# Kernel tuning notes

Hardware: AMD Instinct MI355X
Metric: run time of the kernel (lower is better)

The kernel has to match this reference:

```python
import jax, jax.numpy as jnp
import numpy as np

B, M, N_CTR, K = 16, 2048, 512, 32
DIM, DEPTH, HEADS = 384, 6, 6
EMB = 48  # fourier embedding dim (48//6 = 8 freqs per axis, basis [3,24])


def make_basis():
    e = (2.0 ** np.arange(EMB // 6)).astype(np.float32) * np.pi  # [8]
    z = np.zeros(EMB // 6, np.float32)
    basis = np.stack([np.concatenate([e, z, z]),
                      np.concatenate([z, e, z]),
                      np.concatenate([z, z, e])])  # [3, 24]
    return jnp.asarray(basis)


def fourier_embed(x, basis):
    # x [..., 3] -> [..., 48]  (sin/cos of 24 frequency projections)
    p = jnp.einsum('...d,de->...e', x, basis)
    return jnp.concatenate([jnp.sin(p), jnp.cos(p)], axis=-1)


def fps_idx(pos, n):
    # farthest point sampling, deterministic start at index 0. pos [M,3] -> [n]
    d0 = jnp.sum((pos - pos[0]) ** 2, -1)
    def step(d, _):
        i = jnp.argmax(d)
        d = jnp.minimum(d, jnp.sum((pos - pos[i]) ** 2, -1))
        return d, i
    _, idxs = jax.lax.scan(step, d0, None, length=n - 1)
    return jnp.concatenate([jnp.zeros(1, jnp.int32), idxs.astype(jnp.int32)])


def layernorm(x, g, b, eps=1e-6):
    m = jnp.mean(x, -1, keepdims=True)
    v = jnp.var(x, -1, keepdims=True)
    return (x - m) * jax.lax.rsqrt(v + eps) * g + b


def _lin(key, fi, fo):
    kw, kb = jax.random.split(key)
    w = jax.random.normal(kw, (fi, fo), jnp.float32) / np.sqrt(fi)
    b = jax.random.normal(kb, (fo,), jnp.float32) * 0.01
    return w, b


def setup_inputs() -> dict:
    key = jax.random.key(0)
    ks = jax.random.split(key, 16)
    pc = jax.random.uniform(ks[0], (B, M, 3), jnp.float32)
    embed_w, embed_b = _lin(ks[1], 3 + EMB, DIM)
    lw1, lb1 = _lin(ks[2], 3 + EMB, 256)
    lw2, lb2 = _lin(ks[3], 256, 256)
    gw1, gb1 = _lin(ks[4], 256, 256)
    gw2, gb2 = _lin(ks[5], 256, DIM)
    def stack_lin(k, fi, fo):
        kk = jax.random.split(k, DEPTH)
        ws, bs = zip(*[_lin(kk[i], fi, fo) for i in range(DEPTH)])
        return jnp.stack(ws), jnp.stack(bs)
    qkv_w, qkv_b = stack_lin(ks[6], DIM, 3 * DIM)
    proj_w, proj_b = stack_lin(ks[7], DIM, DIM)
    fc1_w, fc1_b = stack_lin(ks[8], DIM, 4 * DIM)
    fc2_w, fc2_b = stack_lin(ks[9], 4 * DIM, DIM)
    return dict(
        pc=pc, embed_w=embed_w, embed_b=embed_b,
        lw1=lw1, lb1=lb1, lw2=lw2, lb2=lb2,
        gw1=gw1, gb1=gb1, gw2=gw2, gb2=gb2,
        ln1_g=jnp.ones((DEPTH, DIM)), ln1_b=jnp.zeros((DEPTH, DIM)),
        qkv_w=qkv_w, qkv_b=qkv_b, proj_w=proj_w, proj_b=proj_b,
        gamma1=jax.random.normal(ks[10], (DEPTH, DIM)) * 0.1,
        ln2_g=jnp.ones((DEPTH, DIM)), ln2_b=jnp.zeros((DEPTH, DIM)),
        fc1_w=fc1_w, fc1_b=fc1_b, fc2_w=fc2_w, fc2_b=fc2_b,
        gamma2=jax.random.normal(ks[11], (DEPTH, DIM)) * 0.1,
        lnf_g=jnp.ones((DIM,)), lnf_b=jnp.zeros((DIM,)),
    )


def reference(pc, embed_w, embed_b, lw1, lb1, lw2, lb2, gw1, gb1, gw2, gb2,
              ln1_g, ln1_b, qkv_w, qkv_b, proj_w, proj_b, gamma1,
              ln2_g, ln2_b, fc1_w, fc1_b, fc2_w, fc2_b, gamma2, lnf_g, lnf_b):
    basis = make_basis()
    # --- FPS centers (per batch) ---
    idx = jax.vmap(lambda p: fps_idx(p, N_CTR))(pc)                 # [B,N]
    centers = jnp.take_along_axis(pc, idx[:, :, None], axis=1)      # [B,N,3]
    # --- KNN graph: for each center, K nearest of the M points ---
    d2 = jnp.sum((centers[:, :, None, :] - pc[:, None, :, :]) ** 2, -1)  # [B,N,M]
    _, nn_idx = jax.lax.top_k(-d2, K)                               # [B,N,K]
    # --- PointConv: gather -> local MLP -> max-scatter -> global MLP ---
    src = jax.vmap(lambda p, i: p[i])(pc, nn_idx)                   # [B,N,K,3]
    rel = src - centers[:, :, None, :]
    feat = jnp.concatenate([rel, fourier_embed(rel, basis)], -1)    # [B,N,K,51]
    h = jax.nn.relu(feat @ lw1 + lb1) @ lw2 + lb2                   # [B,N,K,256]
    h = jnp.max(h, axis=2)  # scatter_max over edges == max over K neighbors
    x = jax.nn.relu(h @ gw1 + gb1) @ gw2 + gb2                      # [B,N,DIM]
    # --- positional embedding tokens ---
    pe = jnp.concatenate([centers, fourier_embed(centers, basis)], -1) @ embed_w + embed_b
    x = x + pe
    # --- ViT blocks (pre-LN, LayerScale, eval mode: no dropout/droppath) ---
    hd = DIM // HEADS
    scale = hd ** -0.5
    for l in range(DEPTH):
        xn = layernorm(x, ln1_g[l], ln1_b[l])
        qkv = (xn @ qkv_w[l] + qkv_b[l]).reshape(B, N_CTR, 3, HEADS, hd)
        q, k, v = jnp.moveaxis(qkv, 2, 0)                           # [B,N,H,hd]
        att = jax.nn.softmax(jnp.einsum('bqhd,bkhd->bhqk', q, k) * scale, axis=-1)
        o = jnp.einsum('bhqk,bkhd->bqhd', att, v).reshape(B, N_CTR, DIM)
        x = x + gamma1[l] * (o @ proj_w[l] + proj_b[l])
        xn = layernorm(x, ln2_g[l], ln2_b[l])
        mlp = jax.nn.gelu(xn @ fc1_w[l] + fc1_b[l], approximate=False) @ fc2_w[l] + fc2_b[l]
        x = x + gamma2[l] * mlp
    out = layernorm(x, lnf_g, lnf_b)
    return out, centers
```

## Files before the change

### kernel.cpp

```cpp
#include <hip/hip_runtime.h>
#include <math.h>

#define NB 16
#define NM 2048
#define NCTR 512
#define NK 32
#define NDIM 384

typedef unsigned long long ull;
typedef unsigned int uint;
typedef unsigned short ushort;
typedef __attribute__((ext_vector_type(8))) short bf16x8;
typedef __attribute__((ext_vector_type(4))) float f32x4;

__device__ __forceinline__ float dist2_exact(float ax, float ay, float az,
                                             float bx, float by, float bz) {
  float dx = __fsub_rn(ax, bx);
  float dy = __fsub_rn(ay, by);
  float dz = __fsub_rn(az, bz);
  return __fadd_rn(__fadd_rn(__fmul_rn(dx, dx), __fmul_rn(dy, dy)),
                   __fmul_rn(dz, dz));
}

__device__ __forceinline__ float gelu_f(float x) {
  return 0.5f * x * (1.0f + erff(x * 0.70710678118654752f));
}

__device__ __forceinline__ ushort f2bf(float f) {
  uint u = __float_as_uint(f);
  return (ushort)((u + 0x7FFFu + ((u >> 16) & 1u)) >> 16);
}
__device__ __forceinline__ float bf2f(ushort h) {
  return __uint_as_float(((uint)h) << 16);
}

__device__ __forceinline__ void cvt8(float4 p, float4 q, uint4& hi, uint4& lo) {
  float v0 = p.x, v1 = p.y, v2 = p.z, v3 = p.w;
  float v4 = q.x, v5 = q.y, v6 = q.z, v7 = q.w;
  ushort h0 = f2bf(v0), h1 = f2bf(v1), h2 = f2bf(v2), h3 = f2bf(v3);
  ushort h4 = f2bf(v4), h5 = f2bf(v5), h6 = f2bf(v6), h7 = f2bf(v7);
  ushort l0 = f2bf(v0 - bf2f(h0)), l1 = f2bf(v1 - bf2f(h1));
  ushort l2 = f2bf(v2 - bf2f(h2)), l3 = f2bf(v3 - bf2f(h3));
  ushort l4 = f2bf(v4 - bf2f(h4)), l5 = f2bf(v5 - bf2f(h5));
  ushort l6 = f2bf(v6 - bf2f(h6)), l7 = f2bf(v7 - bf2f(h7));
  hi.x = (uint)h0 | ((uint)h1 << 16); hi.y = (uint)h2 | ((uint)h3 << 16);
  hi.z = (uint)h4 | ((uint)h5 << 16); hi.w = (uint)h6 | ((uint)h7 << 16);
  lo.x = (uint)l0 | ((uint)l1 << 16); lo.y = (uint)l2 | ((uint)l3 << 16);
  lo.z = (uint)l4 | ((uint)l5 << 16); lo.w = (uint)l6 | ((uint)l7 << 16);
}

__device__ __forceinline__ void split_store(float v, ushort* H, ushort* L,
                                            size_t off) {
  ushort hi = f2bf(v);
  H[off] = hi;
  L[off] = f2bf(v - bf2f(hi));
}

__device__ __forceinline__ void gload16(const ushort* g, ushort* l) {
  __builtin_amdgcn_global_load_lds(
      (const __attribute__((address_space(1))) void*)g,
      (__attribute__((address_space(3))) void*)l, 16, 0, 0);
}

__global__ __launch_bounds__(256)
void fps_kernel(const float* __restrict__ pc, float* __restrict__ centers) {
  int b = blockIdx.x;
  __shared__ float4 pos4[NM];
  __shared__ ull red[2][4];
  const float* pb = pc + (size_t)b * (NM * 3);
  int tid = threadIdx.x, lane = tid & 63, wv = tid >> 6;
  float px[8], py[8], pz[8];
#pragma unroll
  for (int i = 0; i < 8; ++i) {
    int p = tid + 256 * i;
    float x = pb[3 * p], y = pb[3 * p + 1], z = pb[3 * p + 2];
    px[i] = x; py[i] = y; pz[i] = z;
    pos4[p] = make_float4(x, y, z, 0.f);
  }
  __syncthreads();
  float* cb = centers + (size_t)b * (NCTR * 3);
  float4 s0 = pos4[0];
  float sx = s0.x, sy = s0.y, sz = s0.z;
  if (tid == 0) { cb[0] = sx; cb[1] = sy; cb[2] = sz; }
  float d[8];
  for (int n = 1; n < NCTR; ++n) {
    ull best = 0;
#pragma unroll
    for (int i = 0; i < 8; ++i) {
      int p = tid + 256 * i;
      float nd = dist2_exact(px[i], py[i], pz[i], sx, sy, sz);
      d[i] = (n == 1) ? nd : fminf(d[i], nd);
      ull key = ((ull)__float_as_uint(d[i]) << 32) | (unsigned)(0x7FFFFFFF - p);
      best = best > key ? best : key;
    }
    float dl = __uint_as_float((uint)(best >> 32));
    float wm = dl;
#pragma unroll
    for (int off = 32; off; off >>= 1) wm = fmaxf(wm, __shfl_xor(wm, off));
    ull mask = __ballot(dl == wm);
    ull wkey;
    if (mask & (mask - 1)) {
      wkey = best;
#pragma unroll
      for (int off = 32; off; off >>= 1) {
        ull o = __shfl_xor(wkey, off);
        wkey = wkey > o ? wkey : o;
      }
    } else {
      int src = __ffsll((long long)mask) - 1;
      wkey = __shfl(best, src);
    }
    if (lane == 0) red[n & 1][wv] = wkey;
    __syncthreads();
    ull g0 = red[n & 1][0], g1 = red[n & 1][1];
    ull g2 = red[n & 1][2], g3 = red[n & 1][3];
    ull ga = g0 > g1 ? g0 : g1;
    ull gc2 = g2 > g3 ? g2 : g3;
    ull gb = ga > gc2 ? ga : gc2;
    int j = 0x7FFFFFFF - (int)(unsigned)(gb & 0xFFFFFFFFull);
    float4 np = pos4[j];
    sx = np.x; sy = np.y; sz = np.z;
    if (tid == 0) { cb[n * 3] = sx; cb[n * 3 + 1] = sy; cb[n * 3 + 2] = sz; }
  }
}

__global__ __launch_bounds__(256, 2)
void knn_kernel(const float* __restrict__ pc, const float* __restrict__ centers,
                int* __restrict__ nn) {
  __shared__ float pos[NM * 3];
  int b = blockIdx.x >> 7;
  int n0 = (blockIdx.x & 127) << 2;
  const float* pb = pc + (size_t)b * (NM * 3);
  for (int i = threadIdx.x; i < NM * 3; i += 256) pos[i] = pb[i];
  __syncthreads();
  int wv = threadIdx.x >> 6, lane = threadIdx.x & 63;
  int gc = b * NCTR + n0 + wv;
  float cx = centers[gc * 3], cy = centers[gc * 3 + 1], cz = centers[gc * 3 + 2];
  ull key[32];
  ull gmin[4];
#pragma unroll
  for (int g = 0; g < 4; ++g) {
    gmin[g] = ~0ull;
#pragma unroll
    for (int i = 0; i < 8; ++i) {
      int r = g * 8 + i;
      int p = lane + (r << 6);
      float nd = dist2_exact(pos[3 * p], pos[3 * p + 1], pos[3 * p + 2], cx, cy, cz);
      key[r] = ((ull)__float_as_uint(nd) << 11) | (unsigned)p;
      gmin[g] = gmin[g] < key[r] ? gmin[g] : key[r];
    }
  }
  ull a01 = gmin[0] < gmin[1] ? gmin[0] : gmin[1];
  ull a23 = gmin[2] < gmin[3] ? gmin[2] : gmin[3];
  ull lmin = a01 < a23 ? a01 : a23;
  int* nnc = nn + (size_t)gc * NK;
  for (int round = 0; round < NK; ++round) {
    ull w = lmin;
#pragma unroll
    for (int off = 32; off; off >>= 1) {
      ull o = __shfl_xor(w, off);
      w = w < o ? w : o;
    }
    if (lmin == w) {
      nnc[round] = (int)(w & 2047ull);
#pragma unroll
      for (int g = 0; g < 4; ++g) {
        if (gmin[g] == w) {
          gmin[g] = ~0ull;
#pragma unroll
          for (int i = 0; i < 8; ++i) {
            int r = g * 8 + i;
            key[r] = (key[r] == w) ? ~0ull : key[r];
            gmin[g] = gmin[g] < key[r] ? gmin[g] : key[r];
          }
        }
      }
      ull b01 = gmin[0] < gmin[1] ? gmin[0] : gmin[1];
      ull b23 = gmin[2] < gmin[3] ? gmin[2] : gmin[3];
      lmin = b01 < b23 ? b01 : b23;
    }
  }
}

struct WAll {
  const float* src[8];
  ushort* dst[8];
  int K8[8];
  int N[8];
  int Ksrc[8];
  int blk0[9];
};

__global__ __launch_bounds__(256)
void wconv8(WAll a) {
  int bid = blockIdx.x;
  int f = 0;
#pragma unroll
  for (int i = 1; i < 8; ++i) f += (bid >= a.blk0[i]);
  int K8 = a.K8[f], N = a.N[f], Ksrc = a.Ksrc[f];
  int c = (bid - a.blk0[f]) * 256 + threadIdx.x;
  if (c >= K8 * N) return;
  const float* W = a.src[f];
  ushort* out = a.dst[f];
  int kb = c / N, n = c - kb * N;
  float v[8];
#pragma unroll
  for (int i = 0; i < 8; ++i) {
    int row = kb * 8 + i;
    v[i] = (row < Ksrc) ? W[(size_t)row * N + n] : 0.f;
  }
  float4 p, q;
  p.x = v[0]; p.y = v[1]; p.z = v[2]; p.w = v[3];
  q.x = v[4]; q.y = v[5]; q.z = v[6]; q.w = v[7];
  uint4 hi, lo;
  cvt8(p, q, hi, lo);
  *(uint4*)(out + (size_t)c * 8) = hi;
  *(uint4*)(out + (size_t)(K8 * N + c) * 8) = lo;
}

__global__ __launch_bounds__(256, 2)
void edge_mfma(const float* __restrict__ pc, const float* __restrict__ centers,
               const int* __restrict__ nn, const ushort* __restrict__ lw1s,
               const float* __restrict__ lb1, const ushort* __restrict__ lw2s,
               const float* __restrict__ lb2, ushort* __restrict__ hH,
               ushort* __restrict__ hL) {
  __shared__ __align__(16) ushort featH[4096], featL[4096];
  __shared__ __align__(16) ushort t1H[16384], t1L[16384];
  int tid = threadIdx.x;
  int w = tid >> 6, lane = tid & 63;
  int l15 = lane & 15, l4 = lane >> 4;
  int wbase = w << 6;
  {
    int e = tid >> 2, s = tid & 3;
    int ge = blockIdx.x * 64 + e;
    int c = ge >> 5;
    int b = c >> 9;
    int j = nn[ge];
    const float* sp = pc + ((size_t)b * NM + j) * 3;
    float rx = sp[0] - centers[c * 3];
    float ry = sp[1] - centers[c * 3 + 1];
    float rz = sp[2] - centers[c * 3 + 2];
    auto putk = [&](int k, float v) {
      ushort hi = f2bf(v);
      ushort lo = f2bf(v - bf2f(hi));
      int idx = ((k >> 3) * 64 + e) * 8 + (k & 7);
      featH[idx] = hi;
      featL[idx] = lo;
    };
    if (s < 3) {
      float r = (s == 0) ? rx : (s == 1) ? ry : rz;
#pragma unroll
      for (int f = 0; f < 8; ++f) {
        float ef = (float)(M_PI * (double)(1 << f));
        float p = r * ef;
        putk(3 + 8 * s + f, sinf(p));
        putk(27 + 8 * s + f, cosf(p));
      }
    } else {
      putk(0, rx);
      putk(1, ry);
      putk(2, rz);
#pragma unroll
      for (int k = 51; k < 64; ++k) putk(k, 0.f);
    }
  }
  __syncthreads();
  const ushort* lw1H = lw1s;
  const ushort* lw1L = lw1s + 8 * 256 * 8;
  f32x4 acc1[4][4];
#pragma unroll
  for (int i = 0; i < 4; ++i)
#pragma unroll
    for (int j = 0; j < 4; ++j) acc1[i][j] = (f32x4){0.f, 0.f, 0.f, 0.f};
#pragma unroll
  for (int ks = 0; ks < 2; ++ks) {
    bf16x8 ah[4], al[4];
#pragma unroll
    for (int fm = 0; fm < 4; ++fm) {
      int idx = ((ks * 4 + l4) * 64 + fm * 16 + l15) * 8;
      ah[fm] = *(const bf16x8*)&featH[idx];
      al[fm] = *(const bf16x8*)&featL[idx];
    }
#pragma unroll
    for (int fn = 0; fn < 4; ++fn) {
      int col = wbase + fn * 16 + l15;
      size_t boff = ((size_t)(ks * 4 + l4) * 256 + col) * 8;
      bf16x8 bh = *(const bf16x8*)(lw1H + boff);
      bf16x8 bl = *(const bf16x8*)(lw1L + boff);
#pragma unroll
      for (int fm = 0; fm < 4; ++fm) {
        acc1[fm][fn] = __builtin_amdgcn_mfma_f32_16x16x32_bf16(al[fm], bh, acc1[fm][fn], 0, 0, 0);
        acc1[fm][fn] = __builtin_amdgcn_mfma_f32_16x16x32_bf16(ah[fm], bl, acc1[fm][fn], 0, 0, 0);
        acc1[fm][fn] = __builtin_amdgcn_mfma_f32_16x16x32_bf16(ah[fm], bh, acc1[fm][fn], 0, 0, 0);
      }
    }
  }
#pragma unroll
  for (int fn = 0; fn < 4; ++fn) {
    int chan = wbase + fn * 16 + l15;
    float bias = lb1[chan];
    int kb = chan >> 3, k7 = chan & 7;
#pragma unroll
    for (int fm = 0; fm < 4; ++fm) {
#pragma unroll
      for (int r = 0; r < 4; ++r) {
        int edge = fm * 16 + l4 * 4 + r;
        float v = fmaxf(acc1[fm][fn][r] + bias, 0.f);
        ushort hi = f2bf(v);
        ushort lo = f2bf(v - bf2f(hi));
        int idx = (kb * 64 + edge) * 8 + k7;
        t1H[idx] = hi;
        t1L[idx] = lo;
      }
    }
  }
  __syncthreads();
  const ushort* lw2H = lw2s;
  const ushort* lw2L = lw2s + 32 * 256 * 8;
  f32x4 acc2[4][4];
#pragma unroll
  for (int i = 0; i < 4; ++i)
#pragma unroll
    for (int j = 0; j < 4; ++j) acc2[i][j] = (f32x4){0.f, 0.f, 0.f, 0.f};
#pragma unroll
  for (int ks = 0; ks < 8; ++ks) {
    bf16x8 ah[4], al[4];
#pragma unroll
    for (int fm = 0; fm < 4; ++fm) {
      int idx = ((ks * 4 + l4) * 64 + fm * 16 + l15) * 8;
      ah[fm] = *(const bf16x8*)&t1H[idx];
      al[fm] = *(const bf16x8*)&t1L[idx];
    }
#pragma unroll
    for (int fn = 0; fn < 4; ++fn) {
      int col = wbase + fn * 16 + l15;
      size_t boff = ((size_t)(ks * 4 + l4) * 256 + col) * 8;
      bf16x8 bh = *(const bf16x8*)(lw2H + boff);
      bf16x8 bl = *(const bf16x8*)(lw2L + boff);
#pragma unroll
      for (int fm = 0; fm < 4; ++fm) {
        acc2[fm][fn] = __builtin_amdgcn_mfma_f32_16x16x32_bf16(al[fm], bh, acc2[fm][fn], 0, 0, 0);
        acc2[fm][fn] = __builtin_amdgcn_mfma_f32_16x16x32_bf16(ah[fm], bl, acc2[fm][fn], 0, 0, 0);
        acc2[fm][fn] = __builtin_amdgcn_mfma_f32_16x16x32_bf16(ah[fm], bh, acc2[fm][fn], 0, 0, 0);
      }
    }
  }
#pragma unroll
  for (int fn = 0; fn < 4; ++fn) {
    int col = wbase + fn * 16 + l15;
    float m0 = -INFINITY, m1 = -INFINITY;
#pragma unroll
    for (int r = 0; r < 4; ++r) {
      m0 = fmaxf(m0, fmaxf(acc2[0][fn][r], acc2[1][fn][r]));
      m1 = fmaxf(m1, fmaxf(acc2[2][fn][r], acc2[3][fn][r]));
    }
    m0 = fmaxf(m0, __shfl_xor(m0, 16));
    m0 = fmaxf(m0, __shfl_xor(m0, 32));
    m1 = fmaxf(m1, __shfl_xor(m1, 16));
    m1 = fmaxf(m1, __shfl_xor(m1, 32));
    if (l4 == 0) {
      float bias = lb2[col];
      int c0 = blockIdx.x * 2;
      split_store(m0 + bias, hH, hL, (size_t)c0 * 256 + col);
      split_store(m1 + bias, hH, hL, (size_t)(c0 + 1) * 256 + col);
    }
  }
}

template <int EPI, int OUTS, int BM>
__global__ __launch_bounds__(256, 2)
void gemm_s(const ushort* __restrict__ AH, const ushort* __restrict__ AL,
            const ushort* __restrict__ Wh, const ushort* __restrict__ Wl,
            const float* __restrict__ bias, const float* __restrict__ gamma,
            const float* __restrict__ resid, float* __restrict__ C,
            ushort* __restrict__ CH, ushort* __restrict__ CL,
            int M, int N, int K) {
  constexpr int WC = (BM == 128) ? 2 : 4;
  constexpr int FN = 128 / (WC * 16);
  constexpr int ACH = BM / 64;
  __shared__ __align__(16) ushort Ah[2][BM * 32], Al[2][BM * 32];
  __shared__ __align__(16) ushort Bh[2][4096], Bl[2][4096];
  int tid = threadIdx.x;
  int bn = blockIdx.x << 7, bm = blockIdx.y * BM;
  int wid = tid >> 6, lane = tid & 63;
  int wr = (BM == 128) ? (wid >> 1) : 0;
  int wc = (BM == 128) ? (wid & 1) : wid;
  int l15 = lane & 15, l4 = lane >> 4;

  f32x4 acc[4][FN];
#pragma unroll
  for (int i = 0; i < 4; ++i)
#pragma unroll
    for (int j = 0; j < FN; ++j) acc[i][j] = (f32x4){0.f, 0.f, 0.f, 0.f};

  auto stage = [&](int buf, int kt) {
#pragma unroll
    for (int q = 0; q < ACH; ++q) {
      int e = q * 256 + tid;
      int kb = e / BM, row = e % BM;
      size_t so = (size_t)(bm + row) * K + kt * 32 + kb * 8;
      gload16(AH + so, &Ah[buf][e * 8]);
      gload16(AL + so, &Al[buf][e * 8]);
    }
#pragma unroll
    for (int q = 0; q < 2; ++q) {
      int e = q * 256 + tid;
      int kb = e >> 7, n = e & 127;
      size_t so = ((size_t)(kt * 4 + kb) * N + bn + n) * 8;
      gload16(Wh + so, &Bh[buf][e * 8]);
      gload16(Wl + so, &Bl[buf][e * 8]);
    }
  };

  int nkt = K >> 5;
  stage(0, 0);
  for (int kt = 0; kt < nkt; ++kt) {
    int cur = kt & 1;
    __syncthreads();
    if (kt + 1 < nkt) stage(cur ^ 1, kt + 1);
    bf16x8 ahf[4], alf[4];
#pragma unroll
    for (int fm = 0; fm < 4; ++fm) {
      int ci = l4 * BM + wr * 64 + fm * 16 + l15;
      ahf[fm] = *(bf16x8*)&Ah[cur][ci * 8];
      alf[fm] = *(bf16x8*)&Al[cur][ci * 8];
    }
#pragma unroll
    for (int fn = 0; fn < FN; ++fn) {
      int ci = l4 * 128 + wc * (FN * 16) + fn * 16 + l15;
      bf16x8 bh = *(bf16x8*)&Bh[cur][ci * 8];
      bf16x8 bl = *(bf16x8*)&Bl[cur][ci * 8];
#pragma unroll
      for (int fm = 0; fm < 4; ++fm) {
        acc[fm][fn] = __builtin_amdgcn_mfma_f32_16x16x32_bf16(alf[fm], bh, acc[fm][fn], 0, 0, 0);
        acc[fm][fn] = __builtin_amdgcn_mfma_f32_16x16x32_bf16(ahf[fm], bl, acc[fm][fn], 0, 0, 0);
        acc[fm][fn] = __builtin_amdgcn_mfma_f32_16x16x32_bf16(ahf[fm], bh, acc[fm][fn], 0, 0, 0);
      }
    }
  }

#pragma unroll
  for (int fn = 0; fn < FN; ++fn) {
    int col = bn + wc * (FN * 16) + fn * 16 + l15;
    float bv = bias[col];
    float gv = (EPI == 3) ? gamma[col] : 0.f;
#pragma unroll
    for (int fm = 0; fm < 4; ++fm) {
      int row0 = bm + wr * 64 + fm * 16 + l4 * 4;
#pragma unroll
      for (int r = 0; r < 4; ++r) {
        float v = acc[fm][fn][r] + bv;
        if (EPI == 1) v = fmaxf(v, 0.f);
        else if (EPI == 2) v = gelu_f(v);
        else if (EPI == 3) v = resid[(size_t)(row0 + r) * N + col] + gv * v;
        size_t off = (size_t)(row0 + r) * N + col;
        if (OUTS == 0) C[off] = v;
        else split_store(v, CH, CL, off);
      }
    }
  }
}

__global__ __launch_bounds__(256)
void pe_add(const float* __restrict__ centers, const float* __restrict__ ew,
            const float* __restrict__ eb, float* x) {
  __shared__ float fc[51];
  int c = blockIdx.x, tid = threadIdx.x;
  if (tid < 24) {
    int a = tid >> 3, f = tid & 7;
    float coord = centers[c * 3 + a];
    float p = coord * (float)(M_PI * (double)(1 << f));
    fc[3 + tid] = sinf(p);
    fc[27 + tid] = cosf(p);
  } else if (tid < 27) {
    fc[tid - 24] = centers[c * 3 + (tid - 24)];
  }
  __syncthreads();
  for (int j = tid; j < NDIM; j += 256) {
    float acc = eb[j];
#pragma unroll
    for (int d = 0; d < 51; ++d) acc = fmaf(fc[d], ew[d * NDIM + j], acc);
    x[(size_t)c * NDIM + j] += acc;
  }
}

__global__ __launch_bounds__(256)
void ln_f32(const float* __restrict__ x, const float* __restrict__ g,
            const float* __restrict__ b, float* __restrict__ y) {
  int row = (blockIdx.x << 2) + (threadIdx.x >> 6);
  int lane = threadIdx.x & 63;
  const float* xr = x + (size_t)row * NDIM;
  float v[6];
#pragma unroll
  for (int i = 0; i < 6; ++i) v[i] = xr[lane + (i << 6)];
  float s = 0.f;
#pragma unroll
  for (int i = 0; i < 6; ++i) s += v[i];
#pragma unroll
  for (int off = 32; off; off >>= 1) s += __shfl_xor(s, off);
  float m = s / 384.f;
  float var = 0.f;
#pragma unroll
  for (int i = 0; i < 6; ++i) { float dd = v[i] - m; var += dd * dd; }
#pragma unroll
  for (int off = 32; off; off >>= 1) var += __shfl_xor(var, off);
  var = var / 384.f;
  float rs = 1.f / sqrtf(var + 1e-6f);
#pragma unroll
  for (int i = 0; i < 6; ++i) {
    int cc = lane + (i << 6);
    y[(size_t)row * NDIM + cc] = (v[i] - m) * rs * g[cc] + b[cc];
  }
}

__global__ __launch_bounds__(256)
void ln_split(const float* __restrict__ x, const float* __restrict__ g,
              const float* __restrict__ b, ushort* __restrict__ yH,
              ushort* __restrict__ yL) {
  int row = (blockIdx.x << 2) + (threadIdx.x >> 6);
  int lane = threadIdx.x & 63;
  const float* xr = x + (size_t)row * NDIM;
  float v[6];
#pragma unroll
  for (int i = 0; i < 6; ++i) v[i] = xr[lane + (i << 6)];
  float s = 0.f;
#pragma unroll
  for (int i = 0; i < 6; ++i) s += v[i];
#pragma unroll
  for (int off = 32; off; off >>= 1) s += __shfl_xor(s, off);
  float m = s / 384.f;
  float var = 0.f;
#pragma unroll
  for (int i = 0; i < 6; ++i) { float dd = v[i] - m; var += dd * dd; }
#pragma unroll
  for (int off = 32; off; off >>= 1) var += __shfl_xor(var, off);
  var = var / 384.f;
  float rs = 1.f / sqrtf(var + 1e-6f);
#pragma unroll
  for (int i = 0; i < 6; ++i) {
    int cc = lane + (i << 6);
    float yv = (v[i] - m) * rs * g[cc] + b[cc];
    split_store(yv, yH, yL, (size_t)row * NDIM + cc);
  }
}

__global__ __launch_bounds__(256, 2)
void attn_mfma(const ushort* __restrict__ FH, const ushort* __restrict__ FL,
               ushort* __restrict__ oH, ushort* __restrict__ oL) {
  __shared__ __align__(16) ushort kTH[4096], kTL[4096];
  __shared__ __align__(16) ushort vSH[4096], vSL[4096];
  __shared__ __align__(16) ushort pSH[8192], pSL[8192];
  int bi = blockIdx.x;
  int qt = bi & 3;
  int hh = (bi >> 2) % 6;
  int b = bi / 24;
  int tid = threadIdx.x;
  int w = tid >> 6, lane = tid & 63;
  int l15 = lane & 15, l4 = lane >> 4;
  const ushort* baseH = FH + (size_t)(b * NCTR) * 1152;
  const ushort* baseL = FL + (size_t)(b * NCTR) * 1152;
  int qbase = qt * 128 + w * 32;

  bf16x8 qh[2][2], ql[2][2];
#pragma unroll
  for (int qr = 0; qr < 2; ++qr) {
#pragma unroll
    for (int ds = 0; ds < 2; ++ds) {
      size_t off = (size_t)(qbase + qr * 16 + l15) * 1152 + hh * 64 + ds * 32 + l4 * 8;
      qh[qr][ds] = *(const bf16x8*)(baseH + off);
      ql[qr][ds] = *(const bf16x8*)(baseL + off);
    }
  }

  f32x4 oacc[2][4];
#pragma unroll
  for (int i = 0; i < 2; ++i)
#pragma unroll
    for (int j = 0; j < 4; ++j) oacc[i][j] = (f32x4){0.f, 0.f, 0.f, 0.f};
  float m_[2][4], l_[2][4];
#pragma unroll
  for (int i = 0; i < 2; ++i)
#pragma unroll
    for (int r = 0; r < 4; ++r) { m_[i][r] = -INFINITY; l_[i][r] = 0.f; }

  ushort* pHw = pSH + w * 2048;
  ushort* pLw = pSL + w * 2048;

  for (int ch = 0; ch < 8; ++ch) {
    {
      int key = tid & 63, dgh = tid >> 6;
      size_t krow = (size_t)(ch * 64 + key) * 1152 + 384 + hh * 64;
#pragma unroll
      for (int i = 0; i < 2; ++i) {
        int dg = dgh * 2 + i;
        *(uint4*)&kTH[(dg * 64 + key) * 8] = *(const uint4*)(baseH + krow + dg * 8);
        *(uint4*)&kTL[(dg * 64 + key) * 8] = *(const uint4*)(baseL + krow + dg * 8);
      }
      int d = tid & 63, kb2 = tid >> 6;
#pragma unroll
      for (int i = 0; i < 2; ++i) {
        int kb = kb2 + i * 4;
        ushort hv[8], lv[8];
#pragma unroll
        for (int j = 0; j < 8; ++j) {
          size_t off = (size_t)(ch * 64 + kb * 8 + j) * 1152 + 768 + hh * 64 + d;
          hv[j] = baseH[off];
          lv[j] = baseL[off];
        }
        uint4 H, L;
        H.x = (uint)hv[0] | ((uint)hv[1] << 16); H.y = (uint)hv[2] | ((uint)hv[3] << 16);
        H.z = (uint)hv[4] | ((uint)hv[5] << 16); H.w = (uint)hv[6] | ((uint)hv[7] << 16);
        L.x = (uint)lv[0] | ((uint)lv[1] << 16); L.y = (uint)lv[2] | ((uint)lv[3] << 16);
        L.z = (uint)lv[4] | ((uint)lv[5] << 16); L.w = (uint)lv[6] | ((uint)lv[7] << 16);
        *(uint4*)&vSH[(kb * 64 + d) * 8] = H;
        *(uint4*)&vSL[(kb * 64 + d) * 8] = L;
      }
    }
    __syncthreads();

    f32x4 sacc[2][4];
#pragma unroll
    for (int i = 0; i < 2; ++i)
#pragma unroll
      for (int j = 0; j < 4; ++j) sacc[i][j] = (f32x4){0.f, 0.f, 0.f, 0.f};
#pragma unroll
    for (int ds = 0; ds < 2; ++ds) {
#pragma unroll
      for (int kc = 0; kc < 4; ++kc) {
        int idx = ((ds * 4 + l4) * 64 + kc * 16 + l15) * 8;
        bf16x8 bh = *(const bf16x8*)&kTH[idx];
        bf16x8 bl = *(const bf16x8*)&kTL[idx];
#pragma unroll
        for (int qr = 0; qr < 2; ++qr) {
          sacc[qr][kc] = __builtin_amdgcn_mfma_f32_16x16x32_bf16(ql[qr][ds], bh, sacc[qr][kc], 0, 0, 0);
          sacc[qr][kc] = __builtin_amdgcn_mfma_f32_16x16x32_bf16(qh[qr][ds], bl, sacc[qr][kc], 0, 0, 0);
          sacc[qr][kc] = __builtin_amdgcn_mfma_f32_16x16x32_bf16(qh[qr][ds], bh, sacc[qr][kc], 0, 0, 0);
        }
      }
    }

    float t[2][4];
#pragma unroll
    for (int qr = 0; qr < 2; ++qr)
#pragma unroll
      for (int r = 0; r < 4; ++r) {
        float a0 = sacc[qr][0][r] * 0.125f; sacc[qr][0][r] = a0;
        float a1 = sacc[qr][1][r] * 0.125f; sacc[qr][1][r] = a1;
        float a2 = sacc[qr][2][r] * 0.125f; sacc[qr][2][r] = a2;
        float a3 = sacc[qr][3][r] * 0.125f; sacc[qr][3][r] = a3;
        t[qr][r] = fmaxf(fmaxf(a0, a1), fmaxf(a2, a3));
      }
#pragma unroll
    for (int off = 1; off < 16; off <<= 1)
#pragma unroll
      for (int qr = 0; qr < 2; ++qr)
#pragma unroll
        for (int r = 0; r < 4; ++r)
          t[qr][r] = fmaxf(t[qr][r], __shfl_xor(t[qr][r], off));
    float f_[2][4];
#pragma unroll
    for (int qr = 0; qr < 2; ++qr)
#pragma unroll
      for (int r = 0; r < 4; ++r) {
        float mn = fmaxf(m_[qr][r], t[qr][r]);
        f_[qr][r] = expf(m_[qr][r] - mn);
        m_[qr][r] = mn;
      }
#pragma unroll
    for (int qr = 0; qr < 2; ++qr)
#pragma unroll
      for (int dc = 0; dc < 4; ++dc)
#pragma unroll
        for (int r = 0; r < 4; ++r) oacc[qr][dc][r] *= f_[qr][r];
    float sm[2][4];
#pragma unroll
    for (int qr = 0; qr < 2; ++qr)
#pragma unroll
      for (int r = 0; r < 4; ++r) {
        float p0 = expf(sacc[qr][0][r] - m_[qr][r]); sacc[qr][0][r] = p0;
        float p1 = expf(sacc[qr][1][r] - m_[qr][r]); sacc[qr][1][r] = p1;
        float p2 = expf(sacc[qr][2][r] - m_[qr][r]); sacc[qr][2][r] = p2;
        float p3 = expf(sacc[qr][3][r] - m_[qr][r]); sacc[qr][3][r] = p3;
        sm[qr][r] = ((p0 + p1) + (p2 + p3));
      }
#pragma unroll
    for (int off = 1; off < 16; off <<= 1)
#pragma unroll
      for (int qr = 0; qr < 2; ++qr)
#pragma unroll
        for (int r = 0; r < 4; ++r)
          sm[qr][r] += __shfl_xor(sm[qr][r], off);
#pragma unroll
    for (int qr = 0; qr < 2; ++qr)
#pragma unroll
      for (int r = 0; r < 4; ++r) l_[qr][r] = l_[qr][r] * f_[qr][r] + sm[qr][r];

#pragma unroll
    for (int qr = 0; qr < 2; ++qr)
#pragma unroll
      for (int kc = 0; kc < 4; ++kc)
#pragma unroll
        for (int r = 0; r < 4; ++r) {
          float pv = sacc[qr][kc][r];
          ushort hi = f2bf(pv);
          ushort lo = f2bf(pv - bf2f(hi));
          int k = kc * 16 + l15;
          int qrow = qr * 16 + l4 * 4 + r;
          int idx = ((k >> 3) * 32 + qrow) * 8 + (k & 7);
          pHw[idx] = hi;
          pLw[idx] = lo;
        }

#pragma unroll
    for (int ks = 0; ks < 2; ++ks) {
      bf16x8 pah[2], pal[2];
#pragma unroll
      for (int qr = 0; qr < 2; ++qr) {
        int idx = ((ks * 4 + l4) * 32 + qr * 16 + l15) * 8;
        pah[qr] = *(const bf16x8*)&pHw[idx];
        pal[qr] = *(const bf16x8*)&pLw[idx];
      }
#pragma unroll
      for (int dc = 0; dc < 4; ++dc) {
        int idx = ((ks * 4 + l4) * 64 + dc * 16 + l15) * 8;
        bf16x8 vh = *(const bf16x8*)&vSH[idx];
        bf16x8 vl = *(const bf16x8*)&vSL[idx];
#pragma unroll
        for (int qr = 0; qr < 2; ++qr) {
          oacc[qr][dc] = __builtin_amdgcn_mfma_f32_16x16x32_bf16(pal[qr], vh, oacc[qr][dc], 0, 0, 0);
          oacc[qr][dc] = __builtin_amdgcn_mfma_f32_16x16x32_bf16(pah[qr], vl, oacc[qr][dc], 0, 0, 0);
          oacc[qr][dc] = __builtin_amdgcn_mfma_f32_16x16x32_bf16(pah[qr], vh, oacc[qr][dc], 0, 0, 0);
        }
      }
    }
    __syncthreads();
  }

  float il[2][4];
#pragma unroll
  for (int qr = 0; qr < 2; ++qr)
#pragma unroll
    for (int r = 0; r < 4; ++r) il[qr][r] = 1.f / l_[qr][r];
#pragma unroll
  for (int qr = 0; qr < 2; ++qr)
#pragma unroll
    for (int dc = 0; dc < 4; ++dc)
#pragma unroll
      for (int r = 0; r < 4; ++r) {
        int row = b * NCTR + qbase + qr * 16 + l4 * 4 + r;
        int col = hh * 64 + dc * 16 + l15;
        split_store(oacc[qr][dc][r] * il[qr][r], oH, oL, (size_t)row * NDIM + col);
      }
}

extern "C" void kernel_launch(void* const* d_in, const int* in_sizes, int n_in,
                              void* d_out, int out_size, void* d_ws, size_t ws_size,
                              hipStream_t stream) {
  const float* pc      = (const float*)d_in[0];
  const float* embed_w = (const float*)d_in[1];
  const float* embed_b = (const float*)d_in[2];
  const float* lw1     = (const float*)d_in[3];
  const float* lb1     = (const float*)d_in[4];
  const float* lw2     = (const float*)d_in[5];
  const float* lb2     = (const float*)d_in[6];
  const float* gw1     = (const float*)d_in[7];
  const float* gb1     = (const float*)d_in[8];
  const float* gw2     = (const float*)d_in[9];
  const float* gb2     = (const float*)d_in[10];
  const float* ln1_g   = (const float*)d_in[11];
  const float* ln1_b   = (const float*)d_in[12];
  const float* qkv_w   = (const float*)d_in[13];
  const float* qkv_b   = (const float*)d_in[14];
  const float* proj_w  = (const float*)d_in[15];
  const float* proj_b  = (const float*)d_in[16];
  const float* gamma1  = (const float*)d_in[17];
  const float* ln2_g   = (const float*)d_in[18];
  const float* ln2_b   = (const float*)d_in[19];
  const float* fc1_w   = (const float*)d_in[20];
  const float* fc1_b   = (const float*)d_in[21];
  const float* fc2_w   = (const float*)d_in[22];
  const float* fc2_b   = (const float*)d_in[23];
  const float* gamma2  = (const float*)d_in[24];
  const float* lnf_g   = (const float*)d_in[25];
  const float* lnf_b   = (const float*)d_in[26];

  float* out = (float*)d_out;
  float* centers = out + (size_t)NB * NCTR * NDIM;

  char* ws = (char*)d_ws;
  int*    nn  = (int*)(ws + 0);
  float*  x   = (float*)(ws + 1048576);
  ushort* xnH = (ushort*)(ws + 13631488);
  ushort* xnL = (ushort*)(ws + 19922944);
  ushort* FH  = (ushort*)(ws + 26214400);
  ushort* FL  = (ushort*)(ws + 51380224);
  ushort* hH  = (ushort*)(ws + 76546048);
  ushort* hL  = (ushort*)(ws + 80740352);
  ushort* wsplit = (ushort*)(ws + 84934656);

  WAll wa;
  const float* srcs[8] = {qkv_w, proj_w, fc1_w, fc2_w, gw1, gw2, lw1, lw2};
  int kpads[8] = {2304, 2304, 2304, 9216, 256, 256, 64, 256};
  int ns[8]    = {1152, 384, 1536, 384, 256, 384, 256, 256};
  int ksrcs[8] = {2304, 2304, 2304, 9216, 256, 256, 51, 256};
  ushort* dsts[8];
  size_t wofs = 0;
  int cum = 0;
  for (int f = 0; f < 8; ++f) {
    dsts[f] = wsplit + wofs;
    wofs += (size_t)2 * kpads[f] * ns[f];
    wa.src[f] = srcs[f];
    wa.dst[f] = dsts[f];
    wa.K8[f] = kpads[f] >> 3;
    wa.N[f] = ns[f];
    wa.Ksrc[f] = ksrcs[f];
    wa.blk0[f] = cum;
    cum += ((kpads[f] >> 3) * ns[f] + 255) / 256;
  }
  wa.blk0[8] = cum;
  wconv8<<<cum, 256, 0, stream>>>(wa);
  ushort* qkvS = dsts[0];
  ushort* projS = dsts[1];
  ushort* fc1S = dsts[2];
  ushort* fc2S = dsts[3];
  ushort* g1S = dsts[4];
  ushort* g2S = dsts[5];
  ushort* lw1s = dsts[6];
  ushort* lw2s = dsts[7];

  fps_kernel<<<NB, 256, 0, stream>>>(pc, centers);
  knn_kernel<<<2048, 256, 0, stream>>>(pc, centers, nn);
  edge_mfma<<<4096, 256, 0, stream>>>(pc, centers, nn, lw1s, lb1, lw2s, lb2, hH, hL);

  gemm_s<1, 1, 64><<<dim3(2, 128), 256, 0, stream>>>(
      hH, hL, g1S, g1S + 65536, gb1, nullptr, nullptr, nullptr, xnH, xnL,
      8192, 256, 256);
  gemm_s<0, 0, 64><<<dim3(3, 128), 256, 0, stream>>>(
      xnH, xnL, g2S, g2S + 98304, gb2, nullptr, nullptr, x, nullptr, nullptr,
      8192, 384, 256);
  pe_add<<<8192, 256, 0, stream>>>(centers, embed_w, embed_b, x);

  for (int l = 0; l < 6; ++l) {
    ln_split<<<2048, 256, 0, stream>>>(x, ln1_g + l * 384, ln1_b + l * 384, xnH, xnL);
    gemm_s<0, 1, 128><<<dim3(9, 64), 256, 0, stream>>>(
        xnH, xnL, qkvS + (size_t)l * 442368, qkvS + 2654208 + (size_t)l * 442368,
        qkv_b + l * 1152, nullptr, nullptr, nullptr, FH, FL, 8192, 1152, 384);
    attn_mfma<<<384, 256, 0, stream>>>(FH, FL, xnH, xnL);
    gemm_s<3, 0, 64><<<dim3(3, 128), 256, 0, stream>>>(
        xnH, xnL, projS + (size_t)l * 147456, projS + 884736 + (size_t)l * 147456,
        proj_b + l * 384, gamma1 + l * 384, x, x, nullptr, nullptr, 8192, 384, 384);
    ln_split<<<2048, 256, 0, stream>>>(x, ln2_g + l * 384, ln2_b + l * 384, xnH, xnL);
    gemm_s<2, 1, 128><<<dim3(12, 64), 256, 0, stream>>>(
        xnH, xnL, fc1S + (size_t)l * 589824, fc1S + 3538944 + (size_t)l * 589824,
        fc1_b + l * 1536, nullptr, nullptr, nullptr, FH, FL, 8192, 1536, 384);
    gemm_s<3, 0, 64><<<dim3(3, 128), 256, 0, stream>>>(
        FH, FL, fc2S + (size_t)l * 589824, fc2S + 3538944 + (size_t)l * 589824,
        fc2_b + l * 384, gamma2 + l * 384, x, x, nullptr, nullptr, 8192, 384, 1536);
  }
  ln_f32<<<2048, 256, 0, stream>>>(x, lnf_g, lnf_b, out);
}
```

Baseline: 2.213 ms.

## Merge weight conversion into FPS launch and register-stage GEMM tiles

Weight bf16 hi/lo splitting now runs inside the FPS launch as extra blocks, so the long sequential FPS blocks share the GPU with the conversion blocks and one launch goes away. Separately, the split-bf16 GEMM drops its double-buffered global_load_lds staging in favour of register prefetch into a single LDS buffer, with two barriers per k-step. This halves LDS use, which may let more blocks fit per CU, but it adds a barrier per step and moves staging traffic through VGPRs. The GEMM change hits every transformer layer, so its effect dominates.

```diff
diff --git a/kernel.cpp b/kernel.cpp
--- a/kernel.cpp
+++ b/kernel.cpp
@@ -56,17 +56,47 @@
   L[off] = f2bf(v - bf2f(hi));
 }
 
-__device__ __forceinline__ void gload16(const ushort* g, ushort* l) {
-  __builtin_amdgcn_global_load_lds(
-      (const __attribute__((address_space(1))) void*)g,
-      (__attribute__((address_space(3))) void*)l, 16, 0, 0);
-}
+struct WAll {
+  const float* src[8];
+  ushort* dst[8];
+  int K8[8];
+  int N[8];
+  int Ksrc[8];
+  int blk0[9];
+};
 
 __global__ __launch_bounds__(256)
-void fps_kernel(const float* __restrict__ pc, float* __restrict__ centers) {
-  int b = blockIdx.x;
+void fps_wconv(const float* __restrict__ pc, float* __restrict__ centers,
+               WAll a) {
   __shared__ float4 pos4[NM];
   __shared__ ull red[2][4];
+  if (blockIdx.x >= 16) {
+    int bid = blockIdx.x - 16;
+    int f = 0;
+#pragma unroll
+    for (int i = 1; i < 8; ++i) f += (bid >= a.blk0[i]);
+    int K8 = a.K8[f], N = a.N[f], Ksrc = a.Ksrc[f];
+    int c = (bid - a.blk0[f]) * 256 + threadIdx.x;
+    if (c >= K8 * N) return;
+    const float* W = a.src[f];
+    ushort* out = a.dst[f];
+    int kb = c / N, n = c - kb * N;
+    float v[8];
+#pragma unroll
+    for (int i = 0; i < 8; ++i) {
+      int row = kb * 8 + i;
+      v[i] = (row < Ksrc) ? W[(size_t)row * N + n] : 0.f;
+    }
+    float4 p, q;
+    p.x = v[0]; p.y = v[1]; p.z = v[2]; p.w = v[3];
+    q.x = v[4]; q.y = v[5]; q.z = v[6]; q.w = v[7];
+    uint4 hi, lo;
+    cvt8(p, q, hi, lo);
+    *(uint4*)(out + (size_t)c * 8) = hi;
+    *(uint4*)(out + (size_t)(K8 * N + c) * 8) = lo;
+    return;
+  }
+  int b = blockIdx.x;
   const float* pb = pc + (size_t)b * (NM * 3);
   int tid = threadIdx.x, lane = tid & 63, wv = tid >> 6;
   float px[8], py[8], pz[8];
@@ -180,42 +210,6 @@
       lmin = b01 < b23 ? b01 : b23;
     }
   }
-}
-
-struct WAll {
-  const float* src[8];
-  ushort* dst[8];
-  int K8[8];
-  int N[8];
-  int Ksrc[8];
-  int blk0[9];
-};
-
-__global__ __launch_bounds__(256)
-void wconv8(WAll a) {
-  int bid = blockIdx.x;
-  int f = 0;
-#pragma unroll
-  for (int i = 1; i < 8; ++i) f += (bid >= a.blk0[i]);
-  int K8 = a.K8[f], N = a.N[f], Ksrc = a.Ksrc[f];
-  int c = (bid - a.blk0[f]) * 256 + threadIdx.x;
-  if (c >= K8 * N) return;
-  const float* W = a.src[f];
-  ushort* out = a.dst[f];
-  int kb = c / N, n = c - kb * N;
-  float v[8];
-#pragma unroll
-  for (int i = 0; i < 8; ++i) {
-    int row = kb * 8 + i;
-    v[i] = (row < Ksrc) ? W[(size_t)row * N + n] : 0.f;
-  }
-  float4 p, q;
-  p.x = v[0]; p.y = v[1]; p.z = v[2]; p.w = v[3];
-  q.x = v[4]; q.y = v[5]; q.z = v[6]; q.w = v[7];
-  uint4 hi, lo;
-  cvt8(p, q, hi, lo);
-  *(uint4*)(out + (size_t)c * 8) = hi;
-  *(uint4*)(out + (size_t)(K8 * N + c) * 8) = lo;
 }
 
 __global__ __launch_bounds__(256, 2)
@@ -375,11 +369,9 @@
             const float* __restrict__ resid, float* __restrict__ C,
             ushort* __restrict__ CH, ushort* __restrict__ CL,
             int M, int N, int K) {
-  constexpr int WC = (BM == 128) ? 2 : 4;
-  constexpr int FN = 128 / (WC * 16);
-  constexpr int ACH = BM / 64;
-  __shared__ __align__(16) ushort Ah[2][BM * 32], Al[2][BM * 32];
-  __shared__ __align__(16) ushort Bh[2][4096], Bl[2][4096];
+  constexpr int FN = (BM == 128) ? 4 : 2;
+  __shared__ __align__(16) ushort Ah[BM * 32], Al[BM * 32];
+  __shared__ __align__(16) ushort Bh[4096], Bl[4096];
   int tid = threadIdx.x;
   int bn = blockIdx.x << 7, bm = blockIdx.y * BM;
   int wid = tid >> 6, lane = tid & 63;
@@ -387,49 +379,74 @@
   int wc = (BM == 128) ? (wid & 1) : wid;
   int l15 = lane & 15, l4 = lane >> 4;
 
+  int arow = (BM == 128) ? (tid >> 1) : (tid & 63);
+  int akb0 = (BM == 128) ? ((tid & 1) << 1) : (tid >> 6);
+  const ushort* ApH = AH + (size_t)(bm + arow) * K + akb0 * 8;
+  const ushort* ApL = AL + (size_t)(bm + arow) * K + akb0 * 8;
+  int wkb = tid >> 7, wn = tid & 127;
+
   f32x4 acc[4][FN];
 #pragma unroll
   for (int i = 0; i < 4; ++i)
 #pragma unroll
     for (int j = 0; j < FN; ++j) acc[i][j] = (f32x4){0.f, 0.f, 0.f, 0.f};
 
-  auto stage = [&](int buf, int kt) {
-#pragma unroll
-    for (int q = 0; q < ACH; ++q) {
-      int e = q * 256 + tid;
-      int kb = e / BM, row = e % BM;
-      size_t so = (size_t)(bm + row) * K + kt * 32 + kb * 8;
-      gload16(AH + so, &Ah[buf][e * 8]);
-      gload16(AL + so, &Al[buf][e * 8]);
-    }
-#pragma unroll
-    for (int q = 0; q < 2; ++q) {
-      int e = q * 256 + tid;
-      int kb = e >> 7, n = e & 127;
-      size_t so = ((size_t)(kt * 4 + kb) * N + bn + n) * 8;
-      gload16(Wh + so, &Bh[buf][e * 8]);
-      gload16(Wl + so, &Bl[buf][e * 8]);
-    }
-  };
+  uint4 aH0 = *(const uint4*)(ApH);
+  uint4 aL0 = *(const uint4*)(ApL);
+  uint4 aH1, aL1;
+  if (BM == 128) {
+    aH1 = *(const uint4*)(ApH + 8);
+    aL1 = *(const uint4*)(ApL + 8);
+  }
+  size_t wo1 = ((size_t)wkb * N + bn + wn) * 8;
+  size_t wo2 = ((size_t)(wkb + 2) * N + bn + wn) * 8;
+  uint4 w0 = *(const uint4*)(Wh + wo1);
+  uint4 w1 = *(const uint4*)(Wh + wo2);
+  uint4 w2 = *(const uint4*)(Wl + wo1);
+  uint4 w3 = *(const uint4*)(Wl + wo2);
 
   int nkt = K >> 5;
-  stage(0, 0);
   for (int kt = 0; kt < nkt; ++kt) {
-    int cur = kt & 1;
+    if (BM == 128) {
+      *(uint4*)&Ah[(akb0 * 128 + arow) * 8] = aH0;
+      *(uint4*)&Ah[((akb0 + 1) * 128 + arow) * 8] = aH1;
+      *(uint4*)&Al[(akb0 * 128 + arow) * 8] = aL0;
+      *(uint4*)&Al[((akb0 + 1) * 128 + arow) * 8] = aL1;
+    } else {
+      *(uint4*)&Ah[(akb0 * 64 + arow) * 8] = aH0;
+      *(uint4*)&Al[(akb0 * 64 + arow) * 8] = aL0;
+    }
+    *(uint4*)&Bh[tid * 8] = w0;
+    *(uint4*)&Bh[(tid + 256) * 8] = w1;
+    *(uint4*)&Bl[tid * 8] = w2;
+    *(uint4*)&Bl[(tid + 256) * 8] = w3;
     __syncthreads();
-    if (kt + 1 < nkt) stage(cur ^ 1, kt + 1);
+    if (kt + 1 < nkt) {
+      aH0 = *(const uint4*)(ApH + (kt + 1) * 32);
+      aL0 = *(const uint4*)(ApL + (kt + 1) * 32);
+      if (BM == 128) {
+        aH1 = *(const uint4*)(ApH + (kt + 1) * 32 + 8);
+        aL1 = *(const uint4*)(ApL + (kt + 1) * 32 + 8);
+      }
+      size_t b1 = ((size_t)((kt + 1) * 4 + wkb) * N + bn + wn) * 8;
+      size_t b2 = ((size_t)((kt + 1) * 4 + wkb + 2) * N + bn + wn) * 8;
+      w0 = *(const uint4*)(Wh + b1);
+      w1 = *(const uint4*)(Wh + b2);
+      w2 = *(const uint4*)(Wl + b1);
+      w3 = *(const uint4*)(Wl + b2);
+    }
     bf16x8 ahf[4], alf[4];
 #pragma unroll
     for (int fm = 0; fm < 4; ++fm) {
       int ci = l4 * BM + wr * 64 + fm * 16 + l15;
-      ahf[fm] = *(bf16x8*)&Ah[cur][ci * 8];
-      alf[fm] = *(bf16x8*)&Al[cur][ci * 8];
+      ahf[fm] = *(bf16x8*)&Ah[ci * 8];
+      alf[fm] = *(bf16x8*)&Al[ci * 8];
     }
 #pragma unroll
     for (int fn = 0; fn < FN; ++fn) {
       int ci = l4 * 128 + wc * (FN * 16) + fn * 16 + l15;
-      bf16x8 bh = *(bf16x8*)&Bh[cur][ci * 8];
-      bf16x8 bl = *(bf16x8*)&Bl[cur][ci * 8];
+      bf16x8 bh = *(bf16x8*)&Bh[ci * 8];
+      bf16x8 bl = *(bf16x8*)&Bl[ci * 8];
 #pragma unroll
       for (int fm = 0; fm < 4; ++fm) {
         acc[fm][fn] = __builtin_amdgcn_mfma_f32_16x16x32_bf16(alf[fm], bh, acc[fm][fn], 0, 0, 0);
@@ -437,6 +454,7 @@
         acc[fm][fn] = __builtin_amdgcn_mfma_f32_16x16x32_bf16(ahf[fm], bh, acc[fm][fn], 0, 0, 0);
       }
     }
+    __syncthreads();
   }
 
 #pragma unroll
@@ -818,7 +836,6 @@
     cum += ((kpads[f] >> 3) * ns[f] + 255) / 256;
   }
   wa.blk0[8] = cum;
-  wconv8<<<cum, 256, 0, stream>>>(wa);
   ushort* qkvS = dsts[0];
   ushort* projS = dsts[1];
   ushort* fc1S = dsts[2];
@@ -828,7 +845,7 @@
   ushort* lw1s = dsts[6];
   ushort* lw2s = dsts[7];
 
-  fps_kernel<<<NB, 256, 0, stream>>>(pc, centers);
+  fps_wconv<<<16 + cum, 256, 0, stream>>>(pc, centers, wa);
   knn_kernel<<<2048, 256, 0, stream>>>(pc, centers, nn);
   edge_mfma<<<4096, 256, 0, stream>>>(pc, centers, nn, lw1s, lb1, lw2s, lb2, hH, hL);
 
```

Measured after the change: 1.985 ms, median of 3. 1.12x faster.
